# Kernel optimization log

Hardware: AMD Instinct MI355X
Metric: run time of the kernel (lower is better)

The kernel has to match this reference:

```python
import jax, jax.numpy as jnp
import numpy as np
from jax import lax

N, CI, CO, K, H, W_SP, M = 32, 256, 256, 3, 64, 64, 4
TAU = 1.0 / 30.0
PAD = 1  # spatial-preserving for k=3, stride=1, dilation=1


def setup_inputs() -> dict:
    key = jax.random.key(0)
    ks = jax.random.split(key, 6)
    # kaiming_normal fan_out for the kernel bank: fan_out = CO*K*K (per torch semantics on this 6D tensor layout)
    fan_out = CO * K * K
    std = np.sqrt(2.0 / fan_out)
    x = jax.random.normal(ks[0], (N, CI, H, W_SP), dtype=jnp.float32)
    Wbank = jax.random.normal(ks[1], (CO, M, CI, K, K), dtype=jnp.float32) * std
    Bbank = jnp.zeros((CO, M), dtype=jnp.float32)
    hid = CI // M  # att_fc hidden = in_channels // num_weights
    w1 = jax.random.normal(ks[2], (hid, CI), dtype=jnp.float32) * np.sqrt(1.0 / CI)
    b1 = jnp.zeros((hid,), dtype=jnp.float32)
    w2 = jax.random.normal(ks[3], (M, hid), dtype=jnp.float32) * np.sqrt(1.0 / hid)
    b2 = jnp.zeros((M,), dtype=jnp.float32)
    return {"x": x, "Wbank": Wbank, "Bbank": Bbank, "w1": w1, "b1": b1, "w2": w2, "b2": b2}


def reference(x, Wbank, Bbank, w1, b1, w2, b2):
    n, ci, h, w = x.shape
    co = Wbank.shape[0]
    # attention over kernels: global avg pool -> 1x1 conv MLP -> softmax(logits * tau)
    pooled = jnp.mean(x, axis=(2, 3))                      # N,Ci
    hmid = jax.nn.relu(pooled @ w1.T + b1)                 # N,hid
    logits = hmid @ w2.T + b2                              # N,M
    pi = jax.nn.softmax(logits * TAU, axis=1)              # N,M
    # per-sample aggregated kernels and biases
    wn = jnp.einsum("nm,omikl->noikl", pi, Wbank)          # N,Co,Ci,K,K
    bn = pi @ Bbank.T                                      # N,Co
    # batch-as-groups conv2d (spatial-preserving)
    xg = x.reshape(1, n * ci, h, w)
    wg = wn.reshape(n * co, ci, K, K)
    y = lax.conv_general_dilated(
        xg, wg,
        window_strides=(1, 1),
        padding=[(PAD, PAD), (PAD, PAD)],
        rhs_dilation=(1, 1),
        dimension_numbers=("NCHW", "OIHW", "NCHW"),
        feature_group_count=n,
    )
    y = y.reshape(n, co, h, w) + bn[:, :, None, None]
    return y
```

## Files before the change

### kernel.cpp

```cpp
#include <hip/hip_runtime.h>
#include <hip/hip_bf16.h>
#include <stdint.h>

typedef __bf16 bf16;
typedef __bf16 bf16x8 __attribute__((ext_vector_type(8)));
typedef float f32x4 __attribute__((ext_vector_type(4)));

#define TAU (1.0f/30.0f)

#define NB 32
#define CI 256
#define CO 256
#define HH 64
#define WW 64
#define HID 64

#define WN_ELEMS ((size_t)NB*8*9*16*512)
#define WN_BYTES (WN_ELEMS*2)
#define XB_ELEMS ((size_t)NB*32*64*64*8)
#define XB_BYTES (XB_ELEMS*2)

__device__ __forceinline__ void async16(void* lds_uniform_base, const void* g_perlane) {
  __builtin_amdgcn_global_load_lds(
      (const __attribute__((address_space(1))) uint32_t*)g_perlane,
      (__attribute__((address_space(3))) uint32_t*)lds_uniform_base, 16, 0, 0);
}

__global__ void cvt_pool_kernel(const float* __restrict__ x, bf16* __restrict__ xb,
                                float* __restrict__ pooled) {
  const int cg = blockIdx.x, n = blockIdx.y, tid = threadIdx.x;
  const float* base = x + ((size_t)n*CI + cg*8)*4096;
  bf16* ob = xb + ((size_t)n*32 + cg)*4096*8;
  float s[8];
#pragma unroll
  for (int j = 0; j < 8; ++j) s[j] = 0.f;
  for (int it = 0; it < 16; ++it) {
    int pos = it*256 + tid;
    bf16x8 o;
#pragma unroll
    for (int j = 0; j < 8; ++j) {
      float v = base[(size_t)j*4096 + pos];
      s[j] += v;
      o[j] = (bf16)v;
    }
    *(bf16x8*)(ob + (size_t)pos*8) = o;
  }
  __shared__ float red[4][8];
#pragma unroll
  for (int j = 0; j < 8; ++j)
#pragma unroll
    for (int off = 32; off; off >>= 1) s[j] += __shfl_xor(s[j], off);
  int wv = tid >> 6, lane = tid & 63;
  if (lane == 0)
#pragma unroll
    for (int j = 0; j < 8; ++j) red[wv][j] = s[j];
  __syncthreads();
  if (tid < 8) {
    float t = red[0][tid] + red[1][tid] + red[2][tid] + red[3][tid];
    pooled[n*CI + cg*8 + tid] = t * (1.0f/4096.0f);
  }
}

__global__ void attn_kernel(const float* __restrict__ pooled,
                            const float* __restrict__ w1, const float* __restrict__ b1,
                            const float* __restrict__ w2, const float* __restrict__ b2,
                            float* __restrict__ pi) {
  int n = blockIdx.x, h = threadIdx.x;
  __shared__ float hm[HID];
  __shared__ float lgs[4];
  const float* pr = pooled + n*CI;
  float s = b1[h];
  for (int c = 0; c < CI; ++c) s += pr[c] * w1[h*CI + c];
  hm[h] = s > 0.f ? s : 0.f;
  __syncthreads();
  if (h < 4) {
    float lg = b2[h];
    for (int k = 0; k < HID; ++k) lg += hm[k] * w2[h*HID + k];
    lgs[h] = lg * TAU;
  }
  __syncthreads();
  if (h == 0) {
    float mx = fmaxf(fmaxf(lgs[0], lgs[1]), fmaxf(lgs[2], lgs[3]));
    float e0 = expf(lgs[0]-mx), e1 = expf(lgs[1]-mx), e2 = expf(lgs[2]-mx), e3 = expf(lgs[3]-mx);
    float inv = 1.f / (e0+e1+e2+e3);
    pi[n*4+0] = e0*inv; pi[n*4+1] = e1*inv; pi[n*4+2] = e2*inv; pi[n*4+3] = e3*inv;
  }
}

__global__ void agg_kernel(const float* __restrict__ Wbank, const float* __restrict__ pi,
                           bf16* __restrict__ wn) {
  int wid = blockIdx.x * 4 + (threadIdx.x >> 6);
  int lane = threadIdx.x & 63;
  int c = wid / 144;
  int rem = wid - c*144;
  int kk = rem >> 4;
  int cbg = rem & 15;
  int co  = cbg*16 + (lane & 15);
  int ci0 = c*32 + (lane >> 4)*8;
  float w[4][8];
#pragma unroll
  for (int m = 0; m < 4; ++m)
#pragma unroll
    for (int j = 0; j < 8; ++j)
      w[m][j] = Wbank[(size_t)((co*4 + m)*256 + ci0 + j)*9 + kk];
  for (int n = 0; n < NB; ++n) {
    float p0 = pi[n*4+0], p1 = pi[n*4+1], p2 = pi[n*4+2], p3 = pi[n*4+3];
    bf16x8 o;
#pragma unroll
    for (int j = 0; j < 8; ++j)
      o[j] = (bf16)(p0*w[0][j] + p1*w[1][j] + p2*w[2][j] + p3*w[3][j]);
    *(bf16x8*)(wn + ((size_t)n*1152 + c*144 + kk*16 + cbg)*512 + lane*8) = o;
  }
}

#define XSLOTS (4*6*66)

__global__ __launch_bounds__(256, 2)
void conv_kernel(const bf16* __restrict__ xb, const bf16* __restrict__ wn,
                 const float* __restrict__ pi, const float* __restrict__ Bbank,
                 float* __restrict__ y) {
  __shared__ __align__(16) bf16 xs[XSLOTS*8];
  __shared__ __align__(16) bf16 wa[9*4*512];
  __shared__ float bns[64];
  const int tid = threadIdx.x;
  const int wv = tid >> 6, lane = tid & 63;
  const int hwb = blockIdx.x;
  const int cot = blockIdx.y;
  const int n   = blockIdx.z;
  const int h0 = hwb * 4;

  for (int i = tid; i < XSLOTS*8; i += 256) xs[i] = (bf16)0.f;
  if (tid < 64) {
    int co = cot*64 + tid;
    bns[tid] = pi[n*4+0]*Bbank[co*4+0] + pi[n*4+1]*Bbank[co*4+1]
             + pi[n*4+2]*Bbank[co*4+2] + pi[n*4+3]*Bbank[co*4+3];
  }

  f32x4 acc[4][4];
#pragma unroll
  for (int a = 0; a < 4; ++a)
#pragma unroll
    for (int b = 0; b < 4; ++b)
#pragma unroll
      for (int k = 0; k < 4; ++k) acc[a][b][k] = 0.f;

  const bf16* wnb = wn + (size_t)n * 1152 * 512;
  const int sg = wv;

  for (int c = 0; c < 8; ++c) {
    __syncthreads();
    {
      const bf16* seg = wnb + (size_t)c*144*512 + (size_t)(cot*4 + wv)*512 + lane*8;
#pragma unroll
      for (int kk = 0; kk < 9; ++kk)
        async16(&wa[kk*2048 + wv*512], seg + (size_t)kk*16*512);
    }
    {
      const bf16* xg = xb + ((size_t)(n*32 + c*4 + sg))*4096*8 + lane*8;
#pragma unroll
      for (int r = 0; r < 6; ++r) {
        int hp = h0 - 1 + r;
        if (hp >= 0 && hp < HH)
          async16(&xs[(((sg*6 + r)*66) + 1)*8], xg + (size_t)hp*64*8);
      }
    }
    __syncthreads();
#pragma unroll
    for (int ky = 0; ky < 3; ++ky) {
#pragma unroll
      for (int kx = 0; kx < 3; ++kx) {
        const int kk = ky*3 + kx;
        const int r = wv + ky;
        bf16x8 bfr[4];
#pragma unroll
        for (int f = 0; f < 4; ++f) {
          int wl = f*16 + (lane & 15) + kx;
          bfr[f] = *(const bf16x8*)(&xs[(((lane >> 4)*6 + r)*66 + wl) * 8]);
        }
#pragma unroll
        for (int cb = 0; cb < 4; ++cb) {
          bf16x8 afr = *(const bf16x8*)(&wa[kk*2048 + cb*512 + lane*8]);
#pragma unroll
          for (int f = 0; f < 4; ++f)
            acc[cb][f] = __builtin_amdgcn_mfma_f32_16x16x32_bf16(afr, bfr[f], acc[cb][f], 0, 0, 0);
        }
      }
    }
  }
  const int h = h0 + wv;
#pragma unroll
  for (int cb = 0; cb < 4; ++cb) {
#pragma unroll
    for (int f = 0; f < 4; ++f) {
      const int wcol = f*16 + (lane & 15);
#pragma unroll
      for (int r4 = 0; r4 < 4; ++r4) {
        const int col = cb*16 + (lane >> 4)*4 + r4;
        y[(((size_t)n*CO + cot*64 + col)*HH + h)*WW + wcol] = acc[cb][f][r4] + bns[col];
      }
    }
  }
}

extern "C" void kernel_launch(void* const* d_in, const int* in_sizes, int n_in,
                              void* d_out, int out_size, void* d_ws, size_t ws_size,
                              hipStream_t stream) {
  const float* x     = (const float*)d_in[0];
  const float* Wbank = (const float*)d_in[1];
  const float* Bbank = (const float*)d_in[2];
  const float* w1    = (const float*)d_in[3];
  const float* b1    = (const float*)d_in[4];
  const float* w2    = (const float*)d_in[5];
  const float* b2    = (const float*)d_in[6];
  float* y = (float*)d_out;

  bf16*  wn     = (bf16*)d_ws;
  bf16*  xb     = (bf16*)((char*)d_ws + WN_BYTES);
  float* pooled = (float*)((char*)d_ws + WN_BYTES + XB_BYTES);
  float* pi     = pooled + NB*CI;

  dim3 cg(32, NB);
  cvt_pool_kernel<<<cg, 256, 0, stream>>>(x, xb, pooled);
  attn_kernel<<<NB, HID, 0, stream>>>(pooled, w1, b1, w2, b2, pi);
  agg_kernel<<<288, 256, 0, stream>>>(Wbank, pi, wn);
  dim3 grid(16, 4, NB);
  conv_kernel<<<grid, 256, 0, stream>>>(xb, wn, pi, Bbank, y);
}
```

Baseline: 199.5 us.

## Compute two output rows per wave to reuse weight and input fragments

Each conv block now covers 8 output rows instead of 4, and each wave computes two rows. Input fragments for 4 rows are loaded once per kx and reused across ky, and weight fragments are reused across both rows. This halves the grid and the redundant weight loads from global memory and LDS, and cuts halo overhead. The cost is doubled accumulator registers (128 floats), which may hurt occupancy under launch_bounds(256,2) or cause spills, and fewer blocks to fill the GPU.

```diff
diff --git a/kernel.cpp b/kernel.cpp
--- a/kernel.cpp
+++ b/kernel.cpp
@@ -113,39 +113,42 @@
   }
 }
 
-#define XSLOTS (4*6*66)
+#define XROWS 10
+#define XW 66
 
 __global__ __launch_bounds__(256, 2)
 void conv_kernel(const bf16* __restrict__ xb, const bf16* __restrict__ wn,
                  const float* __restrict__ pi, const float* __restrict__ Bbank,
                  float* __restrict__ y) {
-  __shared__ __align__(16) bf16 xs[XSLOTS*8];
+  __shared__ __align__(16) bf16 xs[4*XROWS*XW*8];
   __shared__ __align__(16) bf16 wa[9*4*512];
   __shared__ float bns[64];
   const int tid = threadIdx.x;
   const int wv = tid >> 6, lane = tid & 63;
+  const int l = lane & 15, u = lane >> 4;
   const int hwb = blockIdx.x;
   const int cot = blockIdx.y;
   const int n   = blockIdx.z;
-  const int h0 = hwb * 4;
-
-  for (int i = tid; i < XSLOTS*8; i += 256) xs[i] = (bf16)0.f;
+  const int h0 = hwb * 8;
+
+  for (int i = tid; i < 4*XROWS*XW*8/8; i += 256) ((int4*)xs)[i] = int4{0,0,0,0};
   if (tid < 64) {
     int co = cot*64 + tid;
     bns[tid] = pi[n*4+0]*Bbank[co*4+0] + pi[n*4+1]*Bbank[co*4+1]
              + pi[n*4+2]*Bbank[co*4+2] + pi[n*4+3]*Bbank[co*4+3];
   }
 
-  f32x4 acc[4][4];
-#pragma unroll
-  for (int a = 0; a < 4; ++a)
-#pragma unroll
-    for (int b = 0; b < 4; ++b)
-#pragma unroll
-      for (int k = 0; k < 4; ++k) acc[a][b][k] = 0.f;
+  f32x4 acc[2][4][4];
+#pragma unroll
+  for (int o = 0; o < 2; ++o)
+#pragma unroll
+    for (int a = 0; a < 4; ++a)
+#pragma unroll
+      for (int b = 0; b < 4; ++b)
+#pragma unroll
+        for (int k = 0; k < 4; ++k) acc[o][a][b][k] = 0.f;
 
   const bf16* wnb = wn + (size_t)n * 1152 * 512;
-  const int sg = wv;
 
   for (int c = 0; c < 8; ++c) {
     __syncthreads();
@@ -156,47 +159,51 @@
         async16(&wa[kk*2048 + wv*512], seg + (size_t)kk*16*512);
     }
     {
-      const bf16* xg = xb + ((size_t)(n*32 + c*4 + sg))*4096*8 + lane*8;
-#pragma unroll
-      for (int r = 0; r < 6; ++r) {
+      const bf16* xg = xb + ((size_t)(n*32 + c*4 + wv))*4096*8 + lane*8;
+#pragma unroll
+      for (int r = 0; r < XROWS; ++r) {
         int hp = h0 - 1 + r;
         if (hp >= 0 && hp < HH)
-          async16(&xs[(((sg*6 + r)*66) + 1)*8], xg + (size_t)hp*64*8);
+          async16(&xs[((wv*XROWS + r)*XW + 1)*8], xg + (size_t)hp*64*8);
       }
     }
     __syncthreads();
 #pragma unroll
-    for (int ky = 0; ky < 3; ++ky) {
-#pragma unroll
-      for (int kx = 0; kx < 3; ++kx) {
+    for (int kx = 0; kx < 3; ++kx) {
+      bf16x8 bfr[4][4];
+#pragma unroll
+      for (int rr = 0; rr < 4; ++rr)
+#pragma unroll
+        for (int f = 0; f < 4; ++f)
+          bfr[rr][f] = *(const bf16x8*)(&xs[((u*XROWS + wv*2 + rr)*XW + f*16 + l + kx)*8]);
+#pragma unroll
+      for (int ky = 0; ky < 3; ++ky) {
         const int kk = ky*3 + kx;
-        const int r = wv + ky;
-        bf16x8 bfr[4];
-#pragma unroll
-        for (int f = 0; f < 4; ++f) {
-          int wl = f*16 + (lane & 15) + kx;
-          bfr[f] = *(const bf16x8*)(&xs[(((lane >> 4)*6 + r)*66 + wl) * 8]);
-        }
 #pragma unroll
         for (int cb = 0; cb < 4; ++cb) {
           bf16x8 afr = *(const bf16x8*)(&wa[kk*2048 + cb*512 + lane*8]);
 #pragma unroll
-          for (int f = 0; f < 4; ++f)
-            acc[cb][f] = __builtin_amdgcn_mfma_f32_16x16x32_bf16(afr, bfr[f], acc[cb][f], 0, 0, 0);
+          for (int o = 0; o < 2; ++o)
+#pragma unroll
+            for (int f = 0; f < 4; ++f)
+              acc[o][cb][f] = __builtin_amdgcn_mfma_f32_16x16x32_bf16(afr, bfr[o+ky][f], acc[o][cb][f], 0, 0, 0);
         }
       }
     }
   }
-  const int h = h0 + wv;
-#pragma unroll
-  for (int cb = 0; cb < 4; ++cb) {
-#pragma unroll
-    for (int f = 0; f < 4; ++f) {
-      const int wcol = f*16 + (lane & 15);
-#pragma unroll
-      for (int r4 = 0; r4 < 4; ++r4) {
-        const int col = cb*16 + (lane >> 4)*4 + r4;
-        y[(((size_t)n*CO + cot*64 + col)*HH + h)*WW + wcol] = acc[cb][f][r4] + bns[col];
+#pragma unroll
+  for (int o = 0; o < 2; ++o) {
+    const int h = h0 + wv*2 + o;
+#pragma unroll
+    for (int cb = 0; cb < 4; ++cb) {
+#pragma unroll
+      for (int f = 0; f < 4; ++f) {
+        const int wcol = f*16 + l;
+#pragma unroll
+        for (int r4 = 0; r4 < 4; ++r4) {
+          const int col = cb*16 + u*4 + r4;
+          y[(((size_t)n*CO + cot*64 + col)*HH + h)*WW + wcol] = acc[o][cb][f][r4] + bns[col];
+        }
       }
     }
   }
@@ -223,6 +230,6 @@
   cvt_pool_kernel<<<cg, 256, 0, stream>>>(x, xb, pooled);
   attn_kernel<<<NB, HID, 0, stream>>>(pooled, w1, b1, w2, b2, pi);
   agg_kernel<<<288, 256, 0, stream>>>(Wbank, pi, wn);
-  dim3 grid(16, 4, NB);
+  dim3 grid(8, 4, NB);
   conv_kernel<<<grid, 256, 0, stream>>>(xb, wn, pi, Bbank, y);
 }
```

Result: faster. 190.4 us (-4.6%).
